# Performance work log

Measured on AMD Instinct MI355X. Metric: run time of the kernel, lower is better.

The kernel has to match this reference:

```python
import jax, jax.numpy as jnp
import numpy as np

B, N, D_IN, D_HID, D_OUT = 64, 512, 512, 512, 512


def setup_inputs() -> dict:
    key = jax.random.key(0)
    ks = jax.random.split(key, 8)
    gain = 0.02  # xavier_normal_ gain used in reset_parameters_xavier

    def xavier(k, fan_in, fan_out):
        std = gain * np.sqrt(2.0 / (fan_in + fan_out))
        return jax.random.normal(k, (fan_in, fan_out), dtype=jnp.float32) * std

    return {
        "batch_graph": jax.random.normal(ks[0], (B, N, D_IN), dtype=jnp.float32),
        "adj": jax.random.uniform(ks[1], (B, N, N), dtype=jnp.float32),
        "W1": xavier(ks[2], D_IN, D_HID),
        "b1": jnp.zeros((D_HID,), dtype=jnp.float32),
        "W2": xavier(ks[3], D_HID, D_HID),
        "b2": jnp.zeros((D_HID,), dtype=jnp.float32),
        "W3": xavier(ks[4], D_HID, D_OUT),
        "b3": jnp.zeros((D_OUT,), dtype=jnp.float32),
    }


def _normalize_adj(adj):
    # rowsum^-0.5 with inf -> 0 (original: torch.pow then isinf mask)
    rowsum = adj.sum(axis=1)                       # [B, N] (sum over dim 1, as in torch)
    safe = jnp.where(rowsum == 0, 1.0, rowsum)
    r = jnp.where(rowsum == 0, 0.0, safe ** -0.5)  # [B, N]
    # (adj @ D)^T @ D = D @ adj^T @ D with D = diag(r)
    return r[:, :, None] * jnp.swapaxes(adj, 1, 2) * r[:, None, :]


def reference(batch_graph, adj, W1, b1, W2, b2, W3, b3):
    # Block-diagonal big_adj @ big_graph == per-graph batched matmul.
    A = _normalize_adj(adj)  # [B, N, N]

    def gc(x, W, b):
        # support = x @ W ; output = A @ support + b
        return jnp.einsum('bij,bjd->bid', A, x @ W) + b

    # dropout is identity in eval mode (deterministic reference)
    x = jax.nn.relu(gc(batch_graph, W1, b1))
    x = jax.nn.relu(gc(x, W2, b2))
    return gc(x, W3, b3)  # [B, N, D_OUT]
```

## Files before the change

kernel.cpp:

```cpp
#include <hip/hip_runtime.h>
#include <cstdint>
#include <cstddef>

typedef _Float16 f16;
typedef _Float16 f16x4 __attribute__((ext_vector_type(4)));
typedef _Float16 f16x8 __attribute__((ext_vector_type(8)));
typedef float    f32x4 __attribute__((ext_vector_type(4)));

#define NB 64
#define NN 262144

__device__ __forceinline__ void gload_lds16(const void* g, void* l) {
    __builtin_amdgcn_global_load_lds(
        (const __attribute__((address_space(1))) void*)g,
        (__attribute__((address_space(3))) void*)l, 16, 0, 0);
}

__global__ void k_cvtX(const float* __restrict__ x, f16* __restrict__ xh) {
    size_t i = ((size_t)blockIdx.x * 256 + threadIdx.x) * 8;
    float4 v0 = *(const float4*)(x + i);
    float4 v1 = *(const float4*)(x + i + 4);
    f16x8 o;
    o[0] = (f16)v0.x; o[1] = (f16)v0.y; o[2] = (f16)v0.z; o[3] = (f16)v0.w;
    o[4] = (f16)v1.x; o[5] = (f16)v1.y; o[6] = (f16)v1.z; o[7] = (f16)v1.w;
    *(f16x8*)(xh + i) = o;
}

__global__ __launch_bounds__(256)
void k_prep(const float* __restrict__ adj, f16* __restrict__ A_raw,
            float* __restrict__ part,
            const float* __restrict__ W1, const float* __restrict__ W2,
            const float* __restrict__ W3, f16* __restrict__ Wt) {
    __shared__ float t[64][68];
    __shared__ float red[4][64];
    const int bid = blockIdx.x, tid = threadIdx.x;
    if (bid < 4096) {
        const int xcd = bid & 7, loc = bid >> 3;
        const int b = xcd * 8 + (loc >> 6);
        const int tile = loc & 63;
        const int i0 = (tile >> 3) * 64, j0 = (tile & 7) * 64;
        const int jt = tile & 7;
        const float* ab = adj + (size_t)b * NN;
        int trow = tid >> 4;
        int tc4  = (tid & 15) * 4;
        #pragma unroll
        for (int s = 0; s < 4; ++s) {
            int rr = trow + s * 16;
            *(f32x4*)&t[rr][tc4] = *(const f32x4*)&ab[(size_t)(j0 + rr) * 512 + i0 + tc4];
        }
        __syncthreads();
        {
            int c = tid & 63, g = tid >> 6;
            float sg = 0.f;
            #pragma unroll
            for (int s = 0; s < 16; ++s) sg += t[g * 16 + s][c];
            red[g][c] = sg;
        }
        f16* Ab = A_raw + (size_t)b * NN;
        int jq = (tid & 15) * 4;
        int ib = tid >> 4;
        #pragma unroll
        for (int s = 0; s < 4; ++s) {
            int ii = ib + s * 16;
            f16x4 o;
            #pragma unroll
            for (int q = 0; q < 4; ++q) o[q] = (f16)t[jq + q][ii];
            *(f16x4*)&Ab[(size_t)(i0 + ii) * 512 + j0 + jq] = o;
        }
        __syncthreads();
        if (tid < 64)
            part[((size_t)b * 8 + jt) * 512 + i0 + tid] =
                red[0][tid] + red[1][tid] + red[2][tid] + red[3][tid];
    } else {
        int cb = bid - 4096;
        int z = cb >> 6, rem = cb & 63;
        const float* W = z == 0 ? W1 : (z == 1 ? W2 : W3);
        f16* out = Wt + (size_t)z * NN;
        int k0 = (rem >> 3) * 64, d0 = (rem & 7) * 64;
        int c = tid & 63, r4 = tid >> 6;
        #pragma unroll
        for (int s = 0; s < 16; ++s) {
            int rr = r4 + s * 4;
            t[rr][c] = W[(size_t)(k0 + rr) * 512 + d0 + c];
        }
        __syncthreads();
        int kq = (tid & 15) * 4;
        int db = tid >> 4;
        #pragma unroll
        for (int s = 0; s < 4; ++s) {
            int dd = db + s * 16;
            f16x4 o;
            #pragma unroll
            for (int q = 0; q < 4; ++q)
                o[q] = (f16)(64.f * t[kq + q][dd]);
            *(f16x4*)&out[(size_t)(d0 + dd) * 512 + k0 + kq] = o;
        }
    }
}

__global__ void k_fin(const float* __restrict__ part, float* __restrict__ r) {
    int idx = blockIdx.x * 256 + threadIdx.x;
    int b = idx >> 9, n = idx & 511;
    const float* p = part + (size_t)b * 8 * 512 + n;
    float s = 0.f;
    #pragma unroll
    for (int jt = 0; jt < 8; ++jt) s += p[jt * 512];
    r[idx] = (s > 0.f) ? rsqrtf(s) : 0.f;
}

template<bool BIAS, bool RELU, bool OUTF32, bool RM, bool RN>
__global__ __launch_bounds__(256, 2)
void gemm_tn_ct(const f16* __restrict__ P, size_t pstr,
                const f16* __restrict__ Qt, size_t qstr,
                void* __restrict__ Cout, size_t cstr,
                const float* __restrict__ bias, const float* __restrict__ rbuf,
                float iscale, float oscale) {
    __shared__ __align__(16) f16 Plds[2][8192];
    __shared__ __align__(16) f16 Qlds[2][8192];

    const int tid  = threadIdx.x;
    const int lane = tid & 63;
    const int wid  = tid >> 6;
    const int wm   = wid >> 1;
    const int wn   = wid & 1;

    const int wg  = blockIdx.x;
    const int swz = (wg & 7) * 128 + (wg >> 3);
    const int b   = swz >> 4;
    const int tt  = swz & 15;
    const int m0  = (tt >> 2) * 128;
    const int n0  = (tt & 3) * 128;

    const f16* Pb = P + (size_t)b * pstr;
    const f16* Qb = Qt + (size_t)b * qstr;
    const float* rs = rbuf + (size_t)b * 512;

    const int srow = tid >> 3;
    const int sswz = (tid & 7) ^ (srow & 7);

    const int fr  = lane & 15;
    const int fs  = lane >> 4;
    const int fx  = fr & 7;

    auto stage = [&](const f16* __restrict__ Gb, int row0, f16* lds, int k0) {
        #pragma unroll
        for (int r = 0; r < 4; ++r) {
            const f16* src = Gb + (size_t)(row0 + r * 32 + srow) * 512 + k0 + sswz * 8;
            gload_lds16(src, lds + r * 2048 + tid * 8);
        }
    };

    f32x4 acc[4][4] = {};

    stage(Pb, m0, &Plds[0][0], 0);
    stage(Qb, n0, &Qlds[0][0], 0);

    for (int t = 0; t < 8; ++t) {
        const int nb = t & 1;
        if (t < 7) {
            stage(Pb, m0, &Plds[nb ^ 1][0], (t + 1) * 64);
            stage(Qb, n0, &Qlds[nb ^ 1][0], (t + 1) * 64);
            asm volatile("s_waitcnt vmcnt(8)" ::: "memory");
        } else {
            asm volatile("s_waitcnt vmcnt(0)" ::: "memory");
        }
        __builtin_amdgcn_s_barrier();

        const f16* Pl = &Plds[nb][0];
        const f16* Ql = &Qlds[nb][0];
        #pragma unroll
        for (int krep = 0; krep < 2; ++krep) {
            const int sp = ((fs + krep * 4) ^ fx) * 8;
            f16x8 af[4], bf[4];
            #pragma unroll
            for (int mi = 0; mi < 4; ++mi)
                af[mi] = *(const f16x8*)&Pl[(wm * 64 + mi * 16 + fr) * 64 + sp];
            #pragma unroll
            for (int ni = 0; ni < 4; ++ni)
                bf[ni] = *(const f16x8*)&Ql[(wn * 64 + ni * 16 + fr) * 64 + sp];
            __builtin_amdgcn_s_setprio(1);
            #pragma unroll
            for (int mi = 0; mi < 4; ++mi)
                #pragma unroll
                for (int ni = 0; ni < 4; ++ni)
                    acc[mi][ni] = __builtin_amdgcn_mfma_f32_16x16x32_f16(
                        af[mi], bf[ni], acc[mi][ni], 0, 0, 0);
            __builtin_amdgcn_s_setprio(0);
        }
        asm volatile("s_waitcnt lgkmcnt(0)" ::: "memory");
        __builtin_amdgcn_sched_barrier(0);
        __builtin_amdgcn_s_barrier();
    }

    const int cmb = (lane >> 4) * 4;
    f32x4 rm4[4];
    float rn1[4];
    if (RM) {
        #pragma unroll
        for (int mi = 0; mi < 4; ++mi)
            rm4[mi] = *(const f32x4*)&rs[m0 + wm * 64 + mi * 16 + cmb];
    }
    if (RN) {
        #pragma unroll
        for (int ni = 0; ni < 4; ++ni)
            rn1[ni] = rs[n0 + wn * 64 + ni * 16 + fr];
    }
    #pragma unroll
    for (int mi = 0; mi < 4; ++mi) {
        #pragma unroll
        for (int ni = 0; ni < 4; ++ni) {
            const int n = n0 + wn * 64 + ni * 16 + fr;
            const int m = m0 + wm * 64 + mi * 16 + cmb;
            float v[4];
            #pragma unroll
            for (int q = 0; q < 4; ++q) {
                float x = acc[mi][ni][q] * iscale;
                if (RM) x *= rm4[mi][q];
                if (RN) x *= rn1[ni];
                if (BIAS) x += bias[m + q];
                if (RELU) x = fmaxf(x, 0.f);
                v[q] = x * oscale;
            }
            if (OUTF32) {
                float* Cb = (float*)Cout + (size_t)b * cstr;
                f32x4 o; o[0] = v[0]; o[1] = v[1]; o[2] = v[2]; o[3] = v[3];
                *(f32x4*)&Cb[(size_t)n * 512 + m] = o;
            } else {
                f16* Cb = (f16*)Cout + (size_t)b * cstr;
                f16x4 o; o[0] = (f16)v[0]; o[1] = (f16)v[1]; o[2] = (f16)v[2]; o[3] = (f16)v[3];
                *(f16x4*)&Cb[(size_t)n * 512 + m] = o;
            }
        }
    }
}

extern "C" void kernel_launch(void* const* d_in, const int* in_sizes, int n_in,
                              void* d_out, int out_size, void* d_ws, size_t ws_size,
                              hipStream_t stream) {
    const float* X0  = (const float*)d_in[0];
    const float* adj = (const float*)d_in[1];
    const float* W1  = (const float*)d_in[2];
    const float* b1  = (const float*)d_in[3];
    const float* W2  = (const float*)d_in[4];
    const float* b2  = (const float*)d_in[5];
    const float* W3  = (const float*)d_in[6];
    const float* b3  = (const float*)d_in[7];

    uint8_t* ws = (uint8_t*)d_ws;
    float* rbuf = (float*)ws;
    f16* Wt1 = (f16*)(ws + 131072);
    f16* Wt2 = Wt1 + NN;
    f16* Wt3 = Wt2 + NN;
    f16* A_raw = (f16*)(ws + 131072 + (size_t)3 * NN * 2);
    f16* Xa  = A_raw + (size_t)NB * NN;
    f16* S_t = Xa + (size_t)NB * NN;
    float* part = (float*)S_t;

    k_prep<<<dim3(4288), dim3(256), 0, stream>>>(adj, A_raw, part, W1, W2, W3, Wt1);
    k_cvtX<<<dim3(8192), dim3(256), 0, stream>>>(X0, Xa);
    k_fin <<<dim3(128),  dim3(256), 0, stream>>>(part, rbuf);

    dim3 gg(1024), gb(256);
    gemm_tn_ct<false, false, false, true,  false><<<gg, gb, 0, stream>>>(Xa,  (size_t)NN, Wt1, (size_t)0,  S_t, (size_t)NN, nullptr, rbuf, 4.f, 1.f);
    gemm_tn_ct<true,  true,  false, false, true ><<<gg, gb, 0, stream>>>(S_t, (size_t)NN, A_raw, (size_t)NN, Xa, (size_t)NN, b1, rbuf, 1.f / 256.f, 256.f);
    gemm_tn_ct<false, false, false, true,  false><<<gg, gb, 0, stream>>>(Xa,  (size_t)NN, Wt2, (size_t)0,  S_t, (size_t)NN, nullptr, rbuf, 16.f, 1.f);
    gemm_tn_ct<true,  true,  false, false, true ><<<gg, gb, 0, stream>>>(S_t, (size_t)NN, A_raw, (size_t)NN, Xa, (size_t)NN, b2, rbuf, 1.f / 262144.f, 256.f);
    gemm_tn_ct<false, false, false, true,  false><<<gg, gb, 0, stream>>>(Xa,  (size_t)NN, Wt3, (size_t)0,  S_t, (size_t)NN, nullptr, rbuf, 16.f, 1.f);
    gemm_tn_ct<true,  false, true,  false, true ><<<gg, gb, 0, stream>>>(S_t, (size_t)NN, A_raw, (size_t)NN, d_out, (size_t)NN, b3, rbuf, 1.f / 262144.f, 1.f);
}
```

Baseline: 219.6 us.

## Fuse six per-layer GEMM launches into one persistent kernel with per-graph barriers

New measurement: 437.5 us. 1.99x slower.

```diff
diff --git a/kernel.cpp b/kernel.cpp
--- a/kernel.cpp
+++ b/kernel.cpp
@@ -98,8 +98,13 @@
     }
 }
 
-__global__ void k_fin(const float* __restrict__ part, float* __restrict__ r) {
+__global__ void k_fin(const float* __restrict__ part, float* __restrict__ r,
+                      uint32_t* __restrict__ syncb) {
     int idx = blockIdx.x * 256 + threadIdx.x;
+    if (blockIdx.x == 0) {
+        syncb[threadIdx.x] = 0;
+        syncb[threadIdx.x + 256] = 0;
+    }
     int b = idx >> 9, n = idx & 511;
     const float* p = part + (size_t)b * 8 * 512 + n;
     float s = 0.f;
@@ -109,38 +114,18 @@
 }
 
 template<bool BIAS, bool RELU, bool OUTF32, bool RM, bool RN>
-__global__ __launch_bounds__(256, 2)
-void gemm_tn_ct(const f16* __restrict__ P, size_t pstr,
-                const f16* __restrict__ Qt, size_t qstr,
-                void* __restrict__ Cout, size_t cstr,
-                const float* __restrict__ bias, const float* __restrict__ rbuf,
-                float iscale, float oscale) {
-    __shared__ __align__(16) f16 Plds[2][8192];
-    __shared__ __align__(16) f16 Qlds[2][8192];
-
+__device__ __forceinline__ void gemm_body(
+    f16* PL, f16* QL,
+    const f16* __restrict__ Pb, const f16* __restrict__ Qb, void* __restrict__ Cb,
+    const float* __restrict__ bias, const float* __restrict__ rs,
+    float iscale, float oscale, int m0, int n0) {
     const int tid  = threadIdx.x;
     const int lane = tid & 63;
     const int wid  = tid >> 6;
-    const int wm   = wid >> 1;
-    const int wn   = wid & 1;
-
-    const int wg  = blockIdx.x;
-    const int swz = (wg & 7) * 128 + (wg >> 3);
-    const int b   = swz >> 4;
-    const int tt  = swz & 15;
-    const int m0  = (tt >> 2) * 128;
-    const int n0  = (tt & 3) * 128;
-
-    const f16* Pb = P + (size_t)b * pstr;
-    const f16* Qb = Qt + (size_t)b * qstr;
-    const float* rs = rbuf + (size_t)b * 512;
-
+    const int wm = wid >> 1, wn = wid & 1;
     const int srow = tid >> 3;
     const int sswz = (tid & 7) ^ (srow & 7);
-
-    const int fr  = lane & 15;
-    const int fs  = lane >> 4;
-    const int fx  = fr & 7;
+    const int fr = lane & 15, fs = lane >> 4, fx = fr & 7;
 
     auto stage = [&](const f16* __restrict__ Gb, int row0, f16* lds, int k0) {
         #pragma unroll
@@ -151,23 +136,22 @@
     };
 
     f32x4 acc[4][4] = {};
-
-    stage(Pb, m0, &Plds[0][0], 0);
-    stage(Qb, n0, &Qlds[0][0], 0);
+    stage(Pb, m0, PL, 0);
+    stage(Qb, n0, QL, 0);
 
     for (int t = 0; t < 8; ++t) {
         const int nb = t & 1;
         if (t < 7) {
-            stage(Pb, m0, &Plds[nb ^ 1][0], (t + 1) * 64);
-            stage(Qb, n0, &Qlds[nb ^ 1][0], (t + 1) * 64);
+            stage(Pb, m0, PL + (nb ^ 1) * 8192, (t + 1) * 64);
+            stage(Qb, n0, QL + (nb ^ 1) * 8192, (t + 1) * 64);
             asm volatile("s_waitcnt vmcnt(8)" ::: "memory");
         } else {
             asm volatile("s_waitcnt vmcnt(0)" ::: "memory");
         }
         __builtin_amdgcn_s_barrier();
 
-        const f16* Pl = &Plds[nb][0];
-        const f16* Ql = &Qlds[nb][0];
+        const f16* Pl = PL + nb * 8192;
+        const f16* Ql = QL + nb * 8192;
         #pragma unroll
         for (int krep = 0; krep < 2; ++krep) {
             const int sp = ((fs + krep * 4) ^ fx) * 8;
@@ -222,14 +206,62 @@
                 v[q] = x * oscale;
             }
             if (OUTF32) {
-                float* Cb = (float*)Cout + (size_t)b * cstr;
                 f32x4 o; o[0] = v[0]; o[1] = v[1]; o[2] = v[2]; o[3] = v[3];
-                *(f32x4*)&Cb[(size_t)n * 512 + m] = o;
+                *(f32x4*)&((float*)Cb)[(size_t)n * 512 + m] = o;
             } else {
-                f16* Cb = (f16*)Cout + (size_t)b * cstr;
                 f16x4 o; o[0] = (f16)v[0]; o[1] = (f16)v[1]; o[2] = (f16)v[2]; o[3] = (f16)v[3];
-                *(f16x4*)&Cb[(size_t)n * 512 + m] = o;
-            }
+                *(f16x4*)&((f16*)Cb)[(size_t)n * 512 + m] = o;
+            }
+        }
+    }
+}
+
+__global__ __launch_bounds__(256, 2)
+void k_mega(f16* __restrict__ Xa, f16* __restrict__ S_t,
+            const f16* __restrict__ A_raw, const f16* __restrict__ Wt,
+            const float* __restrict__ b1, const float* __restrict__ b2,
+            const float* __restrict__ b3, const float* __restrict__ rbuf,
+            float* __restrict__ outp, uint32_t* __restrict__ syncb) {
+    __shared__ __align__(16) f16 Plds[2][8192];
+    __shared__ __align__(16) f16 Qlds[2][8192];
+    const int wg  = blockIdx.x;
+    const int xcd = wg & 7, idx = wg >> 3;
+    const int b   = xcd * 8 + (idx >> 3);
+    const int sub = idx & 7;
+    const int tid = threadIdx.x;
+
+    f16* Xb = Xa + (size_t)b * NN;
+    f16* Sb = S_t + (size_t)b * NN;
+    const f16* Ab = A_raw + (size_t)b * NN;
+    const float* rs = rbuf + (size_t)b * 512;
+    float* Ob = outp + (size_t)b * NN;
+    uint32_t* sc = syncb + b * 8;
+    f16* PL = &Plds[0][0];
+    f16* QL = &Qlds[0][0];
+
+    for (int s = 0; s < 6; ++s) {
+        #pragma unroll 1
+        for (int h = 0; h < 2; ++h) {
+            const int tt = sub * 2 + h;
+            const int m0 = (tt >> 2) * 128, n0 = (tt & 3) * 128;
+            switch (s) {
+            case 0: gemm_body<false, false, false, true,  false>(PL, QL, Xb, Wt,          Sb, nullptr, rs, 4.f,           1.f,   m0, n0); break;
+            case 1: gemm_body<true,  true,  false, false, true >(PL, QL, Sb, Ab,          Xb, b1,      rs, 1.f/256.f,     256.f, m0, n0); break;
+            case 2: gemm_body<false, false, false, true,  false>(PL, QL, Xb, Wt + NN,     Sb, nullptr, rs, 16.f,          1.f,   m0, n0); break;
+            case 3: gemm_body<true,  true,  false, false, true >(PL, QL, Sb, Ab,          Xb, b2,      rs, 1.f/262144.f,  256.f, m0, n0); break;
+            case 4: gemm_body<false, false, false, true,  false>(PL, QL, Xb, Wt + 2*NN,   Sb, nullptr, rs, 16.f,          1.f,   m0, n0); break;
+            case 5: gemm_body<true,  false, true,  false, true >(PL, QL, Sb, Ab,          Ob, b3,      rs, 1.f/262144.f,  1.f,   m0, n0); break;
+            }
+        }
+        if (s < 5) {
+            __syncthreads();
+            if (tid == 0) {
+                __hip_atomic_fetch_add(&sc[s], 1u, __ATOMIC_RELEASE, __HIP_MEMORY_SCOPE_AGENT);
+                while (__hip_atomic_load(&sc[s], __ATOMIC_RELAXED, __HIP_MEMORY_SCOPE_AGENT) < 8u)
+                    __builtin_amdgcn_s_sleep(8);
+            }
+            __syncthreads();
+            __builtin_amdgcn_fence(__ATOMIC_ACQUIRE, "agent");
         }
     }
 }
@@ -249,22 +281,16 @@
     uint8_t* ws = (uint8_t*)d_ws;
     float* rbuf = (float*)ws;
     f16* Wt1 = (f16*)(ws + 131072);
-    f16* Wt2 = Wt1 + NN;
-    f16* Wt3 = Wt2 + NN;
     f16* A_raw = (f16*)(ws + 131072 + (size_t)3 * NN * 2);
     f16* Xa  = A_raw + (size_t)NB * NN;
     f16* S_t = Xa + (size_t)NB * NN;
+    uint32_t* syncb = (uint32_t*)(S_t + (size_t)NB * NN);
     float* part = (float*)S_t;
 
     k_prep<<<dim3(4288), dim3(256), 0, stream>>>(adj, A_raw, part, W1, W2, W3, Wt1);
     k_cvtX<<<dim3(8192), dim3(256), 0, stream>>>(X0, Xa);
-    k_fin <<<dim3(128),  dim3(256), 0, stream>>>(part, rbuf);
-
-    dim3 gg(1024), gb(256);
-    gemm_tn_ct<false, false, false, true,  false><<<gg, gb, 0, stream>>>(Xa,  (size_t)NN, Wt1, (size_t)0,  S_t, (size_t)NN, nullptr, rbuf, 4.f, 1.f);
-    gemm_tn_ct<true,  true,  false, false, true ><<<gg, gb, 0, stream>>>(S_t, (size_t)NN, A_raw, (size_t)NN, Xa, (size_t)NN, b1, rbuf, 1.f / 256.f, 256.f);
-    gemm_tn_ct<false, false, false, true,  false><<<gg, gb, 0, stream>>>(Xa,  (size_t)NN, Wt2, (size_t)0,  S_t, (size_t)NN, nullptr, rbuf, 16.f, 1.f);
-    gemm_tn_ct<true,  true,  false, false, true ><<<gg, gb, 0, stream>>>(S_t, (size_t)NN, A_raw, (size_t)NN, Xa, (size_t)NN, b2, rbuf, 1.f / 262144.f, 256.f);
-    gemm_tn_ct<false, false, false, true,  false><<<gg, gb, 0, stream>>>(Xa,  (size_t)NN, Wt3, (size_t)0,  S_t, (size_t)NN, nullptr, rbuf, 16.f, 1.f);
-    gemm_tn_ct<true,  false, true,  false, true ><<<gg, gb, 0, stream>>>(S_t, (size_t)NN, A_raw, (size_t)NN, d_out, (size_t)NN, b3, rbuf, 1.f / 262144.f, 1.f);
-}
+    k_fin <<<dim3(128),  dim3(256), 0, stream>>>(part, rbuf, syncb);
+
+    k_mega<<<dim3(512), dim3(256), 0, stream>>>(Xa, S_t, A_raw, Wt1, b1, b2, b3,
+                                                rbuf, (float*)d_out, syncb);
+}
```
